# Performance work log

Hardware: AMD Instinct MI355X
Metric: run time of the kernel (lower is better)

The kernel has to match this reference:

```python
import jax, jax.numpy as jnp
import numpy as np

B, T, N = 128, 64, 9
F_IN = 10
D_ENC = 128
HID = 256
H = 4
C = HID // H
EPS = 1e-5


def _build_edges(b, t):
    # chain adjacency + self loops (as in build_graph), then PyG GATv2Conv
    # remove_self_loops before re-adding mean-filled self loops at runtime.
    A = np.zeros((N, N), dtype=bool)
    i = np.arange(N - 1)
    A[i, i + 1] = True
    A[i + 1, i] = True
    A |= np.eye(N, dtype=bool)
    se = np.argwhere(A).T                       # [2, 25]
    e0 = se.shape[1]
    spatial = np.tile(se, (1, t)) + (np.repeat(np.arange(t), e0) * N)[None, :]
    s = np.arange(N * (t - 1))
    temporal = np.stack([s, s + N])             # forward-in-time edges
    single = np.concatenate([spatial, temporal], axis=1)
    eg = single.shape[1]
    ei = np.tile(single, (1, b)) + (np.repeat(np.arange(b), eg) * (t * N))[None, :]
    ei = ei[:, ei[0] != ei[1]]                  # remove_self_loops
    return jnp.asarray(ei[0]), jnp.asarray(ei[1])


def _forward(node_feats, enc_W, enc_b, layers):
    num_nodes = B * T * N
    types = np.array([0] * 7 + [1, 2])
    onehot = np.eye(3, dtype=np.float32)[types]
    dist = np.abs(np.arange(N) - 7).astype(np.float32)  # chain dist to eef (node 7)
    static = jnp.asarray(np.concatenate([onehot, dist[:, None]], axis=1))  # [N,4]
    feats = jnp.concatenate(
        [node_feats, jnp.broadcast_to(static, (B, T, N, 4))], axis=-1)
    # per-node-type encoders (all same dims -> batched einsum)
    x = (jnp.einsum('btnf,ndf->btnd', feats, enc_W) + enc_b).reshape(num_nodes, D_ENC)
    pos = node_feats[..., :3].reshape(num_nodes, 3)
    src, dst = _build_edges(B, T)
    eattr = pos[dst] - pos[src]
    loops = jnp.arange(num_nodes)
    fill = jnp.broadcast_to(eattr.mean(axis=0), (num_nodes, 3))  # fill_value='mean'
    src = jnp.concatenate([src, loops])
    dst = jnp.concatenate([dst, loops])
    eattr = jnp.concatenate([eattr, fill], axis=0)

    for (lW, lb, rW, rb, att, eW, sW, bias, g, b) in layers:
        xl = (x @ lW.T + lb).reshape(num_nodes, H, C)   # source transform
        xr = (x @ rW.T + rb).reshape(num_nodes, H, C)   # target transform
        em = (eattr @ eW.T).reshape(-1, H, C)
        m = jax.nn.leaky_relu(xl[src] + xr[dst] + em, 0.2)
        logit = jnp.einsum('ehc,hc->eh', m, att)        # [E,H]
        lmax = jax.ops.segment_max(logit, dst, num_segments=num_nodes)
        expv = jnp.exp(logit - lmax[dst])
        denom = jax.ops.segment_sum(expv, dst, num_segments=num_nodes)
        w = expv / denom[dst]                           # segment softmax over dst
        out = jax.ops.segment_sum(xl[src] * w[:, :, None], dst,
                                  num_segments=num_nodes)
        x = out.reshape(num_nodes, HID) + x @ sW.T + bias  # residual + bias
        mu = x.mean(-1, keepdims=True)
        var = ((x - mu) ** 2).mean(-1, keepdims=True)
        x = (x - mu) / jnp.sqrt(var + EPS) * g + b      # LayerNorm
        x = x * jax.nn.sigmoid(x)                       # SiLU
    return x.reshape(B, T * N, HID).mean(axis=1)        # global mean pool


def setup_inputs():
    key = jax.random.key(0)
    ks = iter(jax.random.split(key, 64))
    d = {"node_feats": jax.random.normal(next(ks), (B, T, N, F_IN), jnp.float32)}
    d["enc_W"] = jax.random.normal(next(ks), (N, D_ENC, F_IN + 4), jnp.float32) * 0.1
    d["enc_b"] = jnp.zeros((N, D_ENC), jnp.float32)
    dims = [D_ENC, HID, HID]
    for i in range(3):
        din = dims[i]
        d[f"l{i}_lW"] = jax.random.normal(next(ks), (HID, din), jnp.float32) * 0.05
        d[f"l{i}_lb"] = jnp.zeros((HID,), jnp.float32)
        d[f"l{i}_rW"] = jax.random.normal(next(ks), (HID, din), jnp.float32) * 0.05
        d[f"l{i}_rb"] = jnp.zeros((HID,), jnp.float32)
        d[f"l{i}_att"] = jax.random.normal(next(ks), (H, C), jnp.float32) * 0.1
        d[f"l{i}_eW"] = jax.random.normal(next(ks), (HID, 3), jnp.float32) * 0.1
        d[f"l{i}_sW"] = jax.random.normal(next(ks), (HID, din), jnp.float32) * 0.05
        d[f"l{i}_bias"] = jnp.zeros((HID,), jnp.float32)
        d[f"l{i}_g"] = jnp.ones((HID,), jnp.float32)
        d[f"l{i}_b"] = jnp.zeros((HID,), jnp.float32)
    return d


def reference(node_feats, enc_W, enc_b,
              l0_lW, l0_lb, l0_rW, l0_rb, l0_att, l0_eW, l0_sW, l0_bias, l0_g, l0_b,
              l1_lW, l1_lb, l1_rW, l1_rb, l1_att, l1_eW, l1_sW, l1_bias, l1_g, l1_b,
              l2_lW, l2_lb, l2_rW, l2_rb, l2_att, l2_eW, l2_sW, l2_bias, l2_g, l2_b):
    layers = [
        (l0_lW, l0_lb, l0_rW, l0_rb, l0_att, l0_eW, l0_sW, l0_bias, l0_g, l0_b),
        (l1_lW, l1_lb, l1_rW, l1_rb, l1_att, l1_eW, l1_sW, l1_bias, l1_g, l1_b),
        (l2_lW, l2_lb, l2_rW, l2_rb, l2_att, l2_eW, l2_sW, l2_bias, l2_g, l2_b),
    ]
    return _forward(node_feats, enc_W, enc_b, layers)
```

## Files before the change

### kernel.cpp

```cpp
#include <hip/hip_runtime.h>
#include <hip/hip_bf16.h>
#include <math.h>

#define NODES 73728
#define BB    128
#define TT    64
#define NN    9
#define LDX   256
#define E_REAL 203648.0f
#define NARR  33

typedef _Float16 half8 __attribute__((ext_vector_type(8)));
typedef _Float16 half4 __attribute__((ext_vector_type(4)));
typedef float f32x4 __attribute__((ext_vector_type(4)));

__device__ __forceinline__ float bfdec(unsigned short u) {
  return __uint_as_float(((unsigned)u) << 16);
}
__device__ __forceinline__ unsigned short f2h(float x) {
  _Float16 h = (_Float16)x;
  return __builtin_bit_cast(unsigned short, h);
}

#if __has_builtin(__builtin_amdgcn_fdot2)
#define DOT2(a, b, c) __builtin_amdgcn_fdot2((a), (b), (c), false)
#else
#define DOT2(a, b, c) ((c) + (float)(a)[0] * (float)(b)[0] + (float)(a)[1] * (float)(b)[1])
#endif
#define D2(v, k) __builtin_shufflevector((v), (v), 2 * (k), 2 * (k) + 1)

#define MFMA16(a, b, c) __builtin_amdgcn_mfma_f32_16x16x32_f16((a), (b), (c), 0, 0, 0)
#define SB0() __builtin_amdgcn_sched_barrier(0)

__device__ __forceinline__ void gl_lds16(const _Float16* g, _Float16* l) {
  __builtin_amdgcn_global_load_lds(
      (const __attribute__((address_space(1))) void*)g,
      (__attribute__((address_space(3))) void*)l, 16, 0, 0);
}

__global__ __launch_bounds__(256) void detect_kernel(const unsigned short* __restrict__ raw,
                                                     float* __restrict__ flag) {
  __shared__ float sm[256];
  float mx = 0.f;
  for (int i = threadIdx.x; i < 2048; i += 256) mx = fmaxf(mx, fabsf(bfdec(raw[2 * i])));
  sm[threadIdx.x] = mx;
  __syncthreads();
  for (int s = 128; s > 0; s >>= 1) {
    if (threadIdx.x < s) sm[threadIdx.x] = fmaxf(sm[threadIdx.x], sm[threadIdx.x + s]);
    __syncthreads();
  }
  if (threadIdx.x == 0) flag[0] = (sm[0] > 1000.f) ? 1.f : 0.f;
}

struct CvtArgs { const void* src[NARR]; int size[NARR]; int off[NARR]; };

__global__ __launch_bounds__(256) void convert_kernel(CvtArgs a, const float* __restrict__ flag,
                                                      float* __restrict__ dst,
                                                      _Float16* __restrict__ dsth) {
  int i = blockIdx.y;
  int sz = a.size[i];
  bool isf32 = flag[0] > 0.5f;
  const float* sf = (const float*)a.src[i];
  const unsigned short* sh = (const unsigned short*)a.src[i];
  float* d = dst + a.off[i];
  _Float16* dh = dsth + a.off[i];
  for (int j = blockIdx.x * 256 + threadIdx.x; j < sz; j += gridDim.x * 256) {
    float v = isf32 ? sf[j] : bfdec(sh[j]);
    d[j] = v;
    dh[j] = (_Float16)v;
  }
}

__global__ __launch_bounds__(256) void encoder_kernel(const float* __restrict__ nf,
    const float* __restrict__ encW, const float* __restrict__ encb, _Float16* __restrict__ Xh) {
  int tid = threadIdx.x;
  int v = blockIdx.x * 16 + (tid >> 4);
  int d0 = (tid & 15) << 3;
  int n = v % NN;
  float f[14];
#pragma unroll
  for (int i = 0; i < 10; i++) f[i] = nf[(size_t)v * 10 + i];
  f[10] = (n < 7) ? 1.f : 0.f;
  f[11] = (n == 7) ? 1.f : 0.f;
  f[12] = (n == 8) ? 1.f : 0.f;
  f[13] = fabsf((float)(n - 7));
  half8 o;
#pragma unroll
  for (int j = 0; j < 8; j++) {
    int d = d0 + j;
    const float* w = &encW[((size_t)n * 128 + d) * 14];
    float s = encb[n * 128 + d];
#pragma unroll
    for (int i = 0; i < 14; i++) s = fmaf(f[i], w[i], s);
    o[j] = (_Float16)s;
  }
  *(half8*)&Xh[(size_t)v * LDX + d0] = o;
}

__global__ __launch_bounds__(256) void fill_kernel(const float* __restrict__ nf,
                                                   float* __restrict__ fill) {
  __shared__ float sx[256], sy[256], sz[256];
  int tid = threadIdx.x;
  float ax = 0.f, ay = 0.f, az = 0.f;
  for (int p = tid; p < BB * NN; p += 256) {
    int b = p / NN, n = p - b * NN;
    size_t late  = (((size_t)b * TT + (TT - 1)) * NN + n) * 10;
    size_t early = (((size_t)b * TT) * NN + n) * 10;
    ax += nf[late + 0] - nf[early + 0];
    ay += nf[late + 1] - nf[early + 1];
    az += nf[late + 2] - nf[early + 2];
  }
  sx[tid] = ax; sy[tid] = ay; sz[tid] = az;
  __syncthreads();
  for (int s = 128; s > 0; s >>= 1) {
    if (tid < s) { sx[tid] += sx[tid + s]; sy[tid] += sy[tid + s]; sz[tid] += sz[tid + s]; }
    __syncthreads();
  }
  if (tid == 0) { fill[0] = sx[0] / E_REAL; fill[1] = sy[0] / E_REAL; fill[2] = sz[0] / E_REAL; }
}

template <int K>
__global__ __launch_bounds__(512, 4) void fused3_kernel(
    const _Float16* __restrict__ Xin, _Float16* __restrict__ Xout,
    const _Float16* __restrict__ lW, const float* __restrict__ lb,
    const _Float16* __restrict__ rW, const float* __restrict__ rb,
    const _Float16* __restrict__ sW, const float* __restrict__ sb,
    const float* __restrict__ nf, const float* __restrict__ fill,
    const _Float16* __restrict__ atth, const _Float16* __restrict__ ewh,
    const float* __restrict__ gamma, const float* __restrict__ beta,
    float* pool_out, int do_pool) {
  constexpr int NK = K >> 5;
  __shared__ union {
    struct {
      _Float16 B[8 * 3072];
      _Float16 A[3 * NK * 512];
    } loop;
    struct {
      unsigned short xl[50][264];
      unsigned short epi[32][264];
    } s;
    float pacc[8][256];
  } sh;
  int tid = threadIdx.x;
  int row0 = blockIdx.x * 32;
  const int lane = tid & 63, wv = tid >> 6;
  const int quad = lane >> 4, mrow = lane & 15;
  const int bchunk = (lane & 3) ^ ((lane >> 3) & 3);
  const int rchunk = quad ^ ((mrow >> 1) & 3);
  _Float16* ring = sh.loop.B + wv * 3072;
  _Float16* Ald  = sh.loop.A;
  const size_t wcol = (size_t)(wv * 32 + (lane >> 2));
  constexpr size_t wstep = (size_t)16 * K;
  const _Float16* lsrc  = lW + wcol * K + bchunk * 8;
  const _Float16* lsrc2 = lsrc + wstep;
  const _Float16* rsrc  = rW + wcol * K + bchunk * 8;
  const _Float16* rsrc2 = rsrc + wstep;
  const _Float16* ssrc  = sW + wcol * K + bchunk * 8;
  const _Float16* ssrc2 = ssrc + wstep;

  f32x4 accL[3][2] = {};
  f32x4 accR[2][2] = {};
  f32x4 accS[2][2] = {};

  {
    int p = lane >> 2;
    int gnode = (p <= 8) ? (row0 - 9 + p) : (row0 + 32);
    gnode = gnode < 0 ? 0 : (gnode >= NODES ? NODES - 1 : gnode);
    int on0 = row0 + p;
    int on1 = row0 + 16 + p; on1 = on1 >= NODES ? NODES - 1 : on1;
#pragma unroll
    for (int i = 0; i < 3; i++) {
      int c = wv + i * 8;
      if (c < 3 * NK) {
        int t = c / 3, tl = c - t * 3;
        int node = (tl == 0) ? gnode : ((tl == 1) ? on0 : on1);
        gl_lds16(Xin + (size_t)node * LDX + t * 32 + bchunk * 8, Ald + c * 512);
      }
    }
  }
  gl_lds16(lsrc, ring);        gl_lds16(lsrc2, ring + 512);
  gl_lds16(rsrc, ring + 1024); gl_lds16(rsrc2, ring + 1536);
  gl_lds16(ssrc, ring + 2048); gl_lds16(ssrc2, ring + 2560);
  __syncthreads();

#pragma unroll
  for (int t = 0; t < NK; t++) {
    const bool more = (t + 1 < NK);
    const int kn = (t + 1) << 5;
    const _Float16* abase = Ald + (t * 3) * 512 + mrow * 32 + rchunk * 8;
    half8 a0 = *(const half8*)abase;
    half8 a1 = *(const half8*)(abase + 512);
    half8 a2 = *(const half8*)(abase + 1024);
    SB0();
    asm volatile("s_waitcnt vmcnt(4)" ::: "memory");
    SB0();
    {
      half8 b0 = *(const half8*)&ring[(0 * 16 + mrow) * 32 + rchunk * 8];
      half8 b1 = *(const half8*)&ring[(1 * 16 + mrow) * 32 + rchunk * 8];
      accL[0][0] = MFMA16(a0, b0, accL[0][0]);
      accL[0][1] = MFMA16(a0, b1, accL[0][1]);
      accL[1][0] = MFMA16(a1, b0, accL[1][0]);
      accL[1][1] = MFMA16(a1, b1, accL[1][1]);
      accL[2][0] = MFMA16(a2, b0, accL[2][0]);
      accL[2][1] = MFMA16(a2, b1, accL[2][1]);
    }
    SB0();
    if (more) { gl_lds16(lsrc + kn, ring); gl_lds16(lsrc2 + kn, ring + 512); }
    SB0();
    if (more) asm volatile("s_waitcnt vmcnt(4)" ::: "memory");
    else      asm volatile("s_waitcnt vmcnt(2)" ::: "memory");
    SB0();
    {
      const _Float16* bb = ring + 1024;
      half8 b0 = *(const half8*)&bb[(0 * 16 + mrow) * 32 + rchunk * 8];
      half8 b1 = *(const half8*)&bb[(1 * 16 + mrow) * 32 + rchunk * 8];
      accR[0][0] = MFMA16(a1, b0, accR[0][0]);
      accR[1][0] = MFMA16(a2, b0, accR[1][0]);
      accR[0][1] = MFMA16(a1, b1, accR[0][1]);
      accR[1][1] = MFMA16(a2, b1, accR[1][1]);
    }
    SB0();
    if (more) { gl_lds16(rsrc + kn, ring + 1024); gl_lds16(rsrc2 + kn, ring + 1536); }
    SB0();
    if (more) asm volatile("s_waitcnt vmcnt(4)" ::: "memory");
    else      asm volatile("s_waitcnt vmcnt(0)" ::: "memory");
    SB0();
    {
      const _Float16* bb = ring + 2048;
      half8 b0 = *(const half8*)&bb[(0 * 16 + mrow) * 32 + rchunk * 8];
      half8 b1 = *(const half8*)&bb[(1 * 16 + mrow) * 32 + rchunk * 8];
      accS[0][0] = MFMA16(a1, b0, accS[0][0]);
      accS[1][0] = MFMA16(a2, b0, accS[1][0]);
      accS[0][1] = MFMA16(a1, b1, accS[0][1]);
      accS[1][1] = MFMA16(a2, b1, accS[1][1]);
    }
    SB0();
    if (more) { gl_lds16(ssrc + kn, ring + 2048); gl_lds16(ssrc2 + kn, ring + 2560); }
    SB0();
  }

  __syncthreads();

  {
    int quad_ = lane >> 4, mrow_ = lane & 15;
#pragma unroll
    for (int tl = 0; tl < 3; tl++)
#pragma unroll
      for (int ct = 0; ct < 2; ct++) {
        int col = wv * 32 + ct * 16 + mrow_;
        float bs = lb[col];
#pragma unroll
        for (int r = 0; r < 4; r++) {
          int p = quad_ * 4 + r;
          int xlrow;
          if (tl == 0) xlrow = (p <= 8) ? (p + 7) : ((p == 9) ? 48 : 49);
          else         xlrow = tl * 16 + p;
          sh.s.xl[xlrow][col] = f2h(accL[tl][ct][r] + bs);
        }
      }
#pragma unroll
    for (int rt = 0; rt < 2; rt++)
#pragma unroll
      for (int ct = 0; ct < 2; ct++) {
        int col = wv * 32 + ct * 16 + mrow_;
        float bs = rb[col];
#pragma unroll
        for (int r = 0; r < 4; r++)
          sh.s.epi[rt * 16 + quad_ * 4 + r][col] = f2h(accR[rt][ct][r] + bs);
      }
  }
  __syncthreads();

  {
    int g = lane >> 4;
    int l = lane & 15;
    int ch0 = l << 4;
    half8 att_lo = *(const half8*)&atth[ch0];
    half8 att_hi = *(const half8*)&atth[ch0 + 8];
    half8 ew0l, ew1l, ew2l, ew0h, ew1h, ew2h;
#pragma unroll
    for (int j = 0; j < 8; j++) {
      ew0l[j] = ewh[(ch0 + j) * 3 + 0];      ew0h[j] = ewh[(ch0 + 8 + j) * 3 + 0];
      ew1l[j] = ewh[(ch0 + j) * 3 + 1];      ew1h[j] = ewh[(ch0 + 8 + j) * 3 + 1];
      ew2l[j] = ewh[(ch0 + j) * 3 + 2];      ew2h[j] = ewh[(ch0 + 8 + j) * 3 + 2];
    }
    float f0 = fill[0], f1 = fill[1], f2 = fill[2];
    int r = wv * 4 + g;
    int v = row0 + r;
    int n = v % NN;
    int t = (v / NN) & 63;
    int srcs[4] = { v, (n > 0) ? v - 1 : v, (n < NN - 1) ? v + 1 : v, (t > 0) ? v - NN : v };
    bool valid[4] = { true, n > 0, n < NN - 1, t > 0 };
    float px = nf[(size_t)v * 10 + 0];
    float py = nf[(size_t)v * 10 + 1];
    float pz = nf[(size_t)v * 10 + 2];
    _Float16* erow = (_Float16*)sh.s.epi[r];
    half8 xr_lo = *(const half8*)&erow[ch0];
    half8 xr_hi = *(const half8*)&erow[ch0 + 8];
    half8 xls[4][2];
    float lg[4];
#pragma unroll
    for (int e = 0; e < 4; e++) {
      int s = srcs[e];
      float a0, a1, a2;
      if (e == 0) { a0 = f0; a1 = f1; a2 = f2; }
      else {
        a0 = px - nf[(size_t)s * 10 + 0];
        a1 = py - nf[(size_t)s * 10 + 1];
        a2 = pz - nf[(size_t)s * 10 + 2];
      }
      _Float16 h0 = (_Float16)a0, h1 = (_Float16)a1, h2 = (_Float16)a2;
      const _Float16* xrow = (const _Float16*)sh.s.xl[s - row0 + 16];
      xls[e][0] = *(const half8*)&xrow[ch0];
      xls[e][1] = *(const half8*)&xrow[ch0 + 8];
      half8 mlo = (xr_lo + xls[e][0]) + (ew0l * h0 + ew1l * h1 + ew2l * h2);
      half8 mhi = (xr_hi + xls[e][1]) + (ew0h * h0 + ew1h * h1 + ew2h * h2);
      mlo = __builtin_elementwise_max(mlo, mlo * (_Float16)0.2f);
      mhi = __builtin_elementwise_max(mhi, mhi * (_Float16)0.2f);
      float p = 0.f;
      p = DOT2(D2(mlo, 0), D2(att_lo, 0), p);
      p = DOT2(D2(mlo, 1), D2(att_lo, 1), p);
      p = DOT2(D2(mlo, 2), D2(att_lo, 2), p);
      p = DOT2(D2(mlo, 3), D2(att_lo, 3), p);
      p = DOT2(D2(mhi, 0), D2(att_hi, 0), p);
      p = DOT2(D2(mhi, 1), D2(att_hi, 1), p);
      p = DOT2(D2(mhi, 2), D2(att_hi, 2), p);
      p = DOT2(D2(mhi, 3), D2(att_hi, 3), p);
      p += __shfl_xor(p, 1);
      p += __shfl_xor(p, 2);
      lg[e] = valid[e] ? p : -1e30f;
    }
    float mx = fmaxf(fmaxf(lg[0], lg[1]), fmaxf(lg[2], lg[3]));
    float w0 = __expf(lg[0] - mx), w1 = __expf(lg[1] - mx);
    float w2 = __expf(lg[2] - mx), w3 = __expf(lg[3] - mx);
    float inv = 1.f / (w0 + w1 + w2 + w3);
    float wv4[4] = { w0, w1, w2, w3 };
    half8 agg_lo = { 0, 0, 0, 0, 0, 0, 0, 0 };
    half8 agg_hi = { 0, 0, 0, 0, 0, 0, 0, 0 };
#pragma unroll
    for (int e = 0; e < 4; e++) {
      _Float16 wh = (_Float16)(wv4[e] * inv);
      agg_lo = agg_lo + xls[e][0] * wh;
      agg_hi = agg_hi + xls[e][1] * wh;
    }
    *(half8*)&erow[ch0] = agg_lo;
    *(half8*)&erow[ch0 + 8] = agg_hi;
  }
  __syncthreads();

  {
    int quad_ = lane >> 4, mrow_ = lane & 15;
#pragma unroll
    for (int rt = 0; rt < 2; rt++)
#pragma unroll
      for (int ct = 0; ct < 2; ct++) {
        int col = wv * 32 + ct * 16 + mrow_;
        float bs = sb[col];
#pragma unroll
        for (int rr = 0; rr < 4; rr++) {
          int row = rt * 16 + quad_ * 4 + rr;
          _Float16 ag = *(const _Float16*)&sh.s.epi[row][col];
          sh.s.epi[row][col] = f2h(accS[rt][ct][rr] + bs + (float)ag);
        }
      }
  }
  __syncthreads();

  {
    int cc = lane << 2;
    float gm[4], bt[4];
#pragma unroll
    for (int i = 0; i < 4; i++) { gm[i] = gamma[cc + i]; bt[i] = beta[cc + i]; }
    float psum[4] = { 0.f, 0.f, 0.f, 0.f };
    for (int k = 0; k < 4; k++) {
      int r = wv * 4 + k;
      int v = row0 + r;
      const _Float16* erow = (const _Float16*)sh.s.epi[r];
      half4 x4 = *(const half4*)&erow[cc];
      float xv[4] = { (float)x4[0], (float)x4[1], (float)x4[2], (float)x4[3] };
      float s1 = xv[0] + xv[1] + xv[2] + xv[3];
#pragma unroll
      for (int off = 1; off < 64; off <<= 1) s1 += __shfl_xor(s1, off);
      float mu = s1 * (1.f / 256.f);
      float s2 = 0.f;
#pragma unroll
      for (int i = 0; i < 4; i++) { float d = xv[i] - mu; s2 = fmaf(d, d, s2); }
#pragma unroll
      for (int off = 1; off < 64; off <<= 1) s2 += __shfl_xor(s2, off);
      float rs = rsqrtf(s2 * (1.f / 256.f) + 1e-5f);
      half4 o;
#pragma unroll
      for (int i = 0; i < 4; i++) {
        float y = (xv[i] - mu) * rs * gm[i] + bt[i];
        float z = y * (1.f / (1.f + __expf(-y)));
        o[i] = (_Float16)z;
        psum[i] += z;
      }
      *(half4*)&Xout[(size_t)v * LDX + cc] = o;
    }
    if (do_pool) {
      __syncthreads();
#pragma unroll
      for (int i = 0; i < 4; i++) sh.pacc[wv][cc + i] = psum[i];
      __syncthreads();
      if (wv == 0) {
        int b = row0 / 576;
#pragma unroll
        for (int i = 0; i < 4; i++) {
          float s = 0.f;
#pragma unroll
          for (int w = 0; w < 8; w++) s += sh.pacc[w][cc + i];
          atomicAdd(&pool_out[b * 256 + cc + i], s * (1.f / 576.f));
        }
      }
    }
  }
}

extern "C" void kernel_launch(void* const* d_in, const int* in_sizes, int n_in,
                              void* d_out, int out_size, void* d_ws, size_t ws_size,
                              hipStream_t stream) {
  static const int kSize[NARR] = {
    737280, 16128, 1152,
    32768, 256, 32768, 256, 256, 768, 32768, 256, 256, 256,
    65536, 256, 65536, 256, 256, 768, 65536, 256, 256, 256,
    65536, 256, 65536, 256, 256, 768, 65536, 256, 256, 256
  };
  if (n_in != NARR || out_size != BB * 256) return;
  for (int i = 0; i < NARR; i++) if (in_sizes[i] != kSize[i]) return;

  CvtArgs ca;
  int off = 0;
  for (int i = 0; i < NARR; i++) { ca.src[i] = d_in[i]; ca.size[i] = kSize[i]; ca.off[i] = off; off += kSize[i]; }
  const int PRM_ELEMS = off;

  const size_t OFF_FLAG = 0;
  const size_t OFF_FILL = 16;
  const size_t OFF_PRM  = 256;
  const size_t OFF_PRMH = OFF_PRM + (size_t)PRM_ELEMS * 4;
  const size_t OFF_X0   = OFF_PRMH + (size_t)PRM_ELEMS * 2;
  const size_t OFF_X1   = OFF_X0 + (size_t)NODES * LDX * 2;
  const size_t NEED     = OFF_X1 + (size_t)NODES * LDX * 2;
  if (ws_size < NEED) return;

  char* ws = (char*)d_ws;
  float*     flag = (float*)(ws + OFF_FLAG);
  float*     fill = (float*)(ws + OFF_FILL);
  float*     prm  = (float*)(ws + OFF_PRM);
  _Float16*  prmh = (_Float16*)(ws + OFF_PRMH);
  _Float16*  X0   = (_Float16*)(ws + OFF_X0);
  _Float16*  X1   = (_Float16*)(ws + OFF_X1);

  hipMemsetAsync(d_out, 0, (size_t)out_size * 4, stream);
  detect_kernel<<<1, 256, 0, stream>>>((const unsigned short*)d_in[0], flag);
  convert_kernel<<<dim3(128, NARR), 256, 0, stream>>>(ca, flag, prm, prmh);

  const float* nf   = prm + ca.off[0];
  const float* encW = prm + ca.off[1];
  const float* encb = prm + ca.off[2];

  encoder_kernel<<<NODES / 16, 256, 0, stream>>>(nf, encW, encb, X0);
  fill_kernel<<<1, 256, 0, stream>>>(nf, fill);

  _Float16* Xa = X0;
  _Float16* Xb = X1;
  for (int L = 0; L < 3; L++) {
    const _Float16* lWh = prmh + ca.off[3 + L * 10 + 0];
    const float*    lb  = prm  + ca.off[3 + L * 10 + 1];
    const _Float16* rWh = prmh + ca.off[3 + L * 10 + 2];
    const float*    rb  = prm  + ca.off[3 + L * 10 + 3];
    const _Float16* atth= prmh + ca.off[3 + L * 10 + 4];
    const _Float16* ewhp= prmh + ca.off[3 + L * 10 + 5];
    const _Float16* sWh = prmh + ca.off[3 + L * 10 + 6];
    const float*    sb  = prm  + ca.off[3 + L * 10 + 7];
    const float*    g   = prm  + ca.off[3 + L * 10 + 8];
    const float*    b   = prm  + ca.off[3 + L * 10 + 9];
    if (L == 0)
      fused3_kernel<128><<<NODES / 32, 512, 0, stream>>>(Xa, Xb, lWh, lb, rWh, rb, sWh, sb,
                                                         nf, fill, atth, ewhp, g, b,
                                                         (float*)d_out, 0);
    else
      fused3_kernel<256><<<NODES / 32, 512, 0, stream>>>(Xa, Xb, lWh, lb, rWh, rb, sWh, sb,
                                                         nf, fill, atth, ewhp, g, b,
                                                         (float*)d_out, (L == 2) ? 1 : 0);
    _Float16* tmp = Xa; Xa = Xb; Xb = tmp;
  }
}
```

Before: 425.2 us.

## Fuse node encoder into first GAT layer and merge detect with fill

Removes the standalone encoder kernel: layer 0's fused kernel now computes the per-node-type encoder output directly into its swizzled LDS A tile, so encoded features never round-trip through global memory. The fill-mean reduction is folded into the detect kernel, which reads the raw input in either dtype, removing two launches. The cost is redundant encoder compute for halo nodes in each block, plus scalar global weight reads inside layer 0's prologue, which may delay the MFMA pipeline start.

```diff
diff --git a/kernel.cpp b/kernel.cpp
--- a/kernel.cpp
+++ b/kernel.cpp
@@ -38,18 +38,43 @@
       (__attribute__((address_space(3))) void*)l, 16, 0, 0);
 }
 
-__global__ __launch_bounds__(256) void detect_kernel(const unsigned short* __restrict__ raw,
-                                                     float* __restrict__ flag) {
-  __shared__ float sm[256];
+__global__ __launch_bounds__(256) void detect_fill_kernel(const unsigned short* __restrict__ raw,
+                                                          float* __restrict__ flag,
+                                                          float* __restrict__ fill) {
+  __shared__ float sx[256], sy[256], sz[256];
+  int tid = threadIdx.x;
   float mx = 0.f;
-  for (int i = threadIdx.x; i < 2048; i += 256) mx = fmaxf(mx, fabsf(bfdec(raw[2 * i])));
-  sm[threadIdx.x] = mx;
+  for (int i = tid; i < 2048; i += 256) mx = fmaxf(mx, fabsf(bfdec(raw[2 * i])));
+  sx[tid] = mx;
   __syncthreads();
   for (int s = 128; s > 0; s >>= 1) {
-    if (threadIdx.x < s) sm[threadIdx.x] = fmaxf(sm[threadIdx.x], sm[threadIdx.x + s]);
+    if (tid < s) sx[tid] = fmaxf(sx[tid], sx[tid + s]);
     __syncthreads();
   }
-  if (threadIdx.x == 0) flag[0] = (sm[0] > 1000.f) ? 1.f : 0.f;
+  bool isf32 = sx[0] > 1000.f;
+  if (tid == 0) flag[0] = isf32 ? 1.f : 0.f;
+  __syncthreads();
+  const float* rf = (const float*)raw;
+  float ax = 0.f, ay = 0.f, az = 0.f;
+  for (int p = tid; p < BB * NN; p += 256) {
+    int b = p / NN, n = p - b * NN;
+    size_t late  = (((size_t)b * TT + (TT - 1)) * NN + n) * 10;
+    size_t early = (((size_t)b * TT) * NN + n) * 10;
+#pragma unroll
+    for (int i = 0; i < 3; i++) {
+      float lv = isf32 ? rf[late + i]  : bfdec(raw[late + i]);
+      float ev = isf32 ? rf[early + i] : bfdec(raw[early + i]);
+      float d = lv - ev;
+      if (i == 0) ax += d; else if (i == 1) ay += d; else az += d;
+    }
+  }
+  sx[tid] = ax; sy[tid] = ay; sz[tid] = az;
+  __syncthreads();
+  for (int s = 128; s > 0; s >>= 1) {
+    if (tid < s) { sx[tid] += sx[tid + s]; sy[tid] += sy[tid + s]; sz[tid] += sz[tid + s]; }
+    __syncthreads();
+  }
+  if (tid == 0) { fill[0] = sx[0] / E_REAL; fill[1] = sy[0] / E_REAL; fill[2] = sz[0] / E_REAL; }
 }
 
 struct CvtArgs { const void* src[NARR]; int size[NARR]; int off[NARR]; };
@@ -71,55 +96,7 @@
   }
 }
 
-__global__ __launch_bounds__(256) void encoder_kernel(const float* __restrict__ nf,
-    const float* __restrict__ encW, const float* __restrict__ encb, _Float16* __restrict__ Xh) {
-  int tid = threadIdx.x;
-  int v = blockIdx.x * 16 + (tid >> 4);
-  int d0 = (tid & 15) << 3;
-  int n = v % NN;
-  float f[14];
-#pragma unroll
-  for (int i = 0; i < 10; i++) f[i] = nf[(size_t)v * 10 + i];
-  f[10] = (n < 7) ? 1.f : 0.f;
-  f[11] = (n == 7) ? 1.f : 0.f;
-  f[12] = (n == 8) ? 1.f : 0.f;
-  f[13] = fabsf((float)(n - 7));
-  half8 o;
-#pragma unroll
-  for (int j = 0; j < 8; j++) {
-    int d = d0 + j;
-    const float* w = &encW[((size_t)n * 128 + d) * 14];
-    float s = encb[n * 128 + d];
-#pragma unroll
-    for (int i = 0; i < 14; i++) s = fmaf(f[i], w[i], s);
-    o[j] = (_Float16)s;
-  }
-  *(half8*)&Xh[(size_t)v * LDX + d0] = o;
-}
-
-__global__ __launch_bounds__(256) void fill_kernel(const float* __restrict__ nf,
-                                                   float* __restrict__ fill) {
-  __shared__ float sx[256], sy[256], sz[256];
-  int tid = threadIdx.x;
-  float ax = 0.f, ay = 0.f, az = 0.f;
-  for (int p = tid; p < BB * NN; p += 256) {
-    int b = p / NN, n = p - b * NN;
-    size_t late  = (((size_t)b * TT + (TT - 1)) * NN + n) * 10;
-    size_t early = (((size_t)b * TT) * NN + n) * 10;
-    ax += nf[late + 0] - nf[early + 0];
-    ay += nf[late + 1] - nf[early + 1];
-    az += nf[late + 2] - nf[early + 2];
-  }
-  sx[tid] = ax; sy[tid] = ay; sz[tid] = az;
-  __syncthreads();
-  for (int s = 128; s > 0; s >>= 1) {
-    if (tid < s) { sx[tid] += sx[tid + s]; sy[tid] += sy[tid + s]; sz[tid] += sz[tid + s]; }
-    __syncthreads();
-  }
-  if (tid == 0) { fill[0] = sx[0] / E_REAL; fill[1] = sy[0] / E_REAL; fill[2] = sz[0] / E_REAL; }
-}
-
-template <int K>
+template <int K, bool ENC>
 __global__ __launch_bounds__(512, 4) void fused3_kernel(
     const _Float16* __restrict__ Xin, _Float16* __restrict__ Xout,
     const _Float16* __restrict__ lW, const float* __restrict__ lb,
@@ -128,7 +105,8 @@
     const float* __restrict__ nf, const float* __restrict__ fill,
     const _Float16* __restrict__ atth, const _Float16* __restrict__ ewh,
     const float* __restrict__ gamma, const float* __restrict__ beta,
-    float* pool_out, int do_pool) {
+    float* pool_out, int do_pool,
+    const float* __restrict__ encW, const float* __restrict__ encb) {
   constexpr int NK = K >> 5;
   __shared__ union {
     struct {
@@ -162,7 +140,38 @@
   f32x4 accR[2][2] = {};
   f32x4 accS[2][2] = {};
 
-  {
+  if constexpr (ENC) {
+    for (int slot = tid; slot < 3 * NK * 64; slot += 512) {
+      int c = slot >> 6, l = slot & 63;
+      int t = c / 3, tl = c - t * 3;
+      int p = l >> 2, q = l & 3;
+      int d0 = t * 32 + ((q ^ ((p >> 1) & 3)) << 3);
+      int node;
+      if (tl == 0)      node = (p <= 8) ? (row0 - 9 + p) : (row0 + 32);
+      else if (tl == 1) node = row0 + p;
+      else              node = row0 + 16 + p;
+      node = node < 0 ? 0 : (node >= NODES ? NODES - 1 : node);
+      int n = node % NN;
+      float f[14];
+#pragma unroll
+      for (int i = 0; i < 10; i++) f[i] = nf[(size_t)node * 10 + i];
+      f[10] = (n < 7) ? 1.f : 0.f;
+      f[11] = (n == 7) ? 1.f : 0.f;
+      f[12] = (n == 8) ? 1.f : 0.f;
+      f[13] = fabsf((float)(n - 7));
+      half8 o;
+#pragma unroll
+      for (int j = 0; j < 8; j++) {
+        int d = d0 + j;
+        const float* w = &encW[((size_t)n * 128 + d) * 14];
+        float s = encb[n * 128 + d];
+#pragma unroll
+        for (int i = 0; i < 14; i++) s = fmaf(f[i], w[i], s);
+        o[j] = (_Float16)s;
+      }
+      *(half8*)(Ald + c * 512 + p * 32 + q * 8) = o;
+    }
+  } else {
     int p = lane >> 2;
     int gnode = (p <= 8) ? (row0 - 9 + p) : (row0 + 32);
     gnode = gnode < 0 ? 0 : (gnode >= NODES ? NODES - 1 : gnode);
@@ -452,18 +461,13 @@
   _Float16*  X1   = (_Float16*)(ws + OFF_X1);
 
   hipMemsetAsync(d_out, 0, (size_t)out_size * 4, stream);
-  detect_kernel<<<1, 256, 0, stream>>>((const unsigned short*)d_in[0], flag);
+  detect_fill_kernel<<<1, 256, 0, stream>>>((const unsigned short*)d_in[0], flag, fill);
   convert_kernel<<<dim3(128, NARR), 256, 0, stream>>>(ca, flag, prm, prmh);
 
   const float* nf   = prm + ca.off[0];
   const float* encW = prm + ca.off[1];
   const float* encb = prm + ca.off[2];
 
-  encoder_kernel<<<NODES / 16, 256, 0, stream>>>(nf, encW, encb, X0);
-  fill_kernel<<<1, 256, 0, stream>>>(nf, fill);
-
-  _Float16* Xa = X0;
-  _Float16* Xb = X1;
   for (int L = 0; L < 3; L++) {
     const _Float16* lWh = prmh + ca.off[3 + L * 10 + 0];
     const float*    lb  = prm  + ca.off[3 + L * 10 + 1];
@@ -476,13 +480,16 @@
     const float*    g   = prm  + ca.off[3 + L * 10 + 8];
     const float*    b   = prm  + ca.off[3 + L * 10 + 9];
     if (L == 0)
-      fused3_kernel<128><<<NODES / 32, 512, 0, stream>>>(Xa, Xb, lWh, lb, rWh, rb, sWh, sb,
-                                                         nf, fill, atth, ewhp, g, b,
-                                                         (float*)d_out, 0);
+      fused3_kernel<128, true><<<NODES / 32, 512, 0, stream>>>(
+          X1 , X0, lWh, lb, rWh, rb, sWh, sb, nf, fill, atth, ewhp, g, b,
+          (float*)d_out, 0, encW, encb);
+    else if (L == 1)
+      fused3_kernel<256, false><<<NODES / 32, 512, 0, stream>>>(
+          X0, X1, lWh, lb, rWh, rb, sWh, sb, nf, fill, atth, ewhp, g, b,
+          (float*)d_out, 0, nullptr, nullptr);
     else
-      fused3_kernel<256><<<NODES / 32, 512, 0, stream>>>(Xa, Xb, lWh, lb, rWh, rb, sWh, sb,
-                                                         nf, fill, atth, ewhp, g, b,
-                                                         (float*)d_out, (L == 2) ? 1 : 0);
-    _Float16* tmp = Xa; Xa = Xb; Xb = tmp;
-  }
-}
+      fused3_kernel<256, false><<<NODES / 32, 512, 0, stream>>>(
+          X1, X0, lWh, lb, rWh, rb, sWh, sb, nf, fill, atth, ewhp, g, b,
+          (float*)d_out, 1, nullptr, nullptr);
+  }
+}
```

New measurement: 416.1 us. -2.1%, faster.
